# Kernel tuning notes

Measured on AMD Instinct MI355X. Metric: run time of the kernel, lower is better.

Reference implementation:

```python
import jax, jax.numpy as jnp
import numpy as np

B, N, D = 2048, 65536, 128  # batch queries, max_engrams, spike_dim


def setup_inputs() -> dict:
    key = jax.random.key(0)
    k1, k2, k3, k4 = jax.random.split(key, 4)
    sensor_spikes = jax.random.normal(k1, (B, D), dtype=jnp.float32)
    # crystallize_skill stores sign(pattern), so keys/values are +-1 vectors
    sensor_keys = jnp.sign(jax.random.normal(k2, (N, D), dtype=jnp.float32))
    action_values = jnp.sign(jax.random.normal(k3, (N, D), dtype=jnp.float32))
    is_active = jax.random.bernoulli(k4, 0.5, (N,))
    return {
        "sensor_spikes": sensor_spikes,
        "sensor_keys": sensor_keys,
        "action_values": action_values,
        "is_active": is_active,
    }


def reference(sensor_spikes, sensor_keys, action_values, is_active):
    # similarity = x @ keys.T  -> [B, N]
    sim = jnp.einsum("bd,nd->bn", sensor_spikes.astype(jnp.float32), sensor_keys)
    # masked_fill_(~is_active, -inf)
    sim = jnp.where(is_active[None, :], sim, -jnp.inf)
    best_match_idx = jnp.argmax(sim, axis=-1)          # [B]
    confidence = jnp.max(sim, axis=-1)                 # [B] == sim[b, best_idx[b]]
    retrieved = action_values[best_match_idx]          # [B, D]
    return retrieved, confidence, best_match_idx
```

## Files before the change

### kernel.cpp

```cpp
#include <hip/hip_runtime.h>
#include <stdint.h>

typedef __attribute__((ext_vector_type(8))) short short8;
typedef __attribute__((ext_vector_type(4))) float f32x4;

#define NEG_INF (-__builtin_inff())

#define B_ROWS 2048
#define N_KEYS 65536
#define DIM    128
#define NCHUNK 2048


__device__ __forceinline__ unsigned short f2bf(float f) {
  unsigned u = __float_as_uint(f);
  u = (u + 0x7FFFu + ((u >> 16) & 1u)) >> 16;
  return (unsigned short)u;
}


__global__ __launch_bounds__(256) void convert_x_kernel(
    const float* __restrict__ x, short8* __restrict__ xi) {
  int t = blockIdx.x * 256 + threadIdx.x;
  int rb = t >> 8, loc = t & 255;
  int rl = rb * 16 + (loc & 15);
  int c = loc >> 4;
  const float* src = x + (size_t)rl * DIM + c * 8;
  f32x4 v0 = *(const f32x4*)(src);
  f32x4 v1 = *(const f32x4*)(src + 4);
  short8 o;
  o[0] = (short)f2bf(v0[0]); o[1] = (short)f2bf(v0[1]);
  o[2] = (short)f2bf(v0[2]); o[3] = (short)f2bf(v0[3]);
  o[4] = (short)f2bf(v1[0]); o[5] = (short)f2bf(v1[1]);
  o[6] = (short)f2bf(v1[2]); o[7] = (short)f2bf(v1[3]);
  xi[t] = o;
}

__global__ __launch_bounds__(256, 4) void sim4_kernel(
    const short8* __restrict__ xi, const float* __restrict__ keys,
    const int* __restrict__ act, float* __restrict__ cmax) {
  __shared__ short8 Bs[2048];
  const int tid = threadIdx.x;
  const int w = tid >> 6, l = tid & 63;
  const int ntile = blockIdx.x;

  const float* kb = keys + (size_t)ntile * (128 * DIM);
#pragma unroll
  for (int it = 0; it < 8; ++it) {
    int li = it * 256 + tid;
    int rl = ((li >> 8) << 4) + (li & 15);
    int c = (li >> 4) & 15;
    const float* src = kb + rl * DIM + c * 8;
    f32x4 v0 = *(const f32x4*)(src);
    f32x4 v1 = *(const f32x4*)(src + 4);
    int a = act[ntile * 128 + rl];
    short8 o;
    o[0] = (short)f2bf(v0[0]); o[1] = (short)f2bf(v0[1]);
    o[2] = (short)f2bf(v0[2]); o[3] = (short)f2bf(v0[3]);
    o[4] = (short)f2bf(v1[0]); o[5] = (short)f2bf(v1[1]);
    o[6] = (short)f2bf(v1[2]); o[7] = (short)f2bf(v1[3]);
    if (!a) o = short8{0, 0, 0, 0, 0, 0, 0, 0};
    Bs[li] = o;
  }
  __syncthreads();

  short8 kf[2][4];
#pragma unroll
  for (int mi = 0; mi < 2; mi++)
#pragma unroll
    for (int kk = 0; kk < 4; kk++)
      kf[mi][kk] = Bs[(w * 2 + mi) * 256 + kk * 64 + l];

  const int chunk = ntile * 4 + w;
  const int lr = l & 15;
  float* cbase = cmax + chunk;

  for (int it = 0; it < 64; ++it) {
    short8 xf[2][4];
#pragma unroll
    for (int ni = 0; ni < 2; ni++)
#pragma unroll
      for (int kk = 0; kk < 4; kk++)
        xf[ni][kk] = xi[(it * 2 + ni) * 256 + kk * 64 + l];

    f32x4 acc[2][2];
#pragma unroll
    for (int mi = 0; mi < 2; mi++)
#pragma unroll
      for (int ni = 0; ni < 2; ni++) acc[mi][ni] = f32x4{0.f, 0.f, 0.f, 0.f};

#pragma unroll
    for (int kk = 0; kk < 4; kk++)
#pragma unroll
      for (int mi = 0; mi < 2; mi++)
#pragma unroll
        for (int ni = 0; ni < 2; ni++)
          acc[mi][ni] = __builtin_amdgcn_mfma_f32_16x16x32_bf16(
              kf[mi][kk], xf[ni][kk], acc[mi][ni], 0, 0, 0);

#pragma unroll
    for (int ni = 0; ni < 2; ni++) {
      float t0 = fmaxf(acc[0][ni][0], acc[1][ni][0]);
      float t1 = fmaxf(acc[0][ni][1], acc[1][ni][1]);
      float t2 = fmaxf(acc[0][ni][2], acc[1][ni][2]);
      float t3 = fmaxf(acc[0][ni][3], acc[1][ni][3]);
      float v = fmaxf(fmaxf(t0, t1), fmaxf(t2, t3));
      v = fmaxf(v, __shfl_xor(v, 16));
      v = fmaxf(v, __shfl_xor(v, 32));
      if (l < 16)
        cbase[(size_t)(it * 32 + ni * 16 + lr) * NCHUNK] = v;
    }
  }
}

__global__ __launch_bounds__(256) void finalize2_kernel(
    const float* __restrict__ x, const float* __restrict__ keys,
    const float* __restrict__ vals, const int* __restrict__ act,
    const float* __restrict__ cmax, float* __restrict__ out) {
  __shared__ float xr[128];
  __shared__ float wred[4];
  __shared__ int cand[256];
  __shared__ int ncand;
  __shared__ double redv[4];
  __shared__ int redn[4];
  __shared__ int bestn_s;
  const int b = blockIdx.x, tid = threadIdx.x;
  const int w = tid >> 6, l = tid & 63;
  if (tid < 128) xr[tid] = x[(size_t)b * 128 + tid];
  if (tid == 0) ncand = 0;
  __syncthreads();

  const float* cm = cmax + (size_t)b * NCHUNK;
  float c[8];
  float lm = NEG_INF;
#pragma unroll
  for (int j = 0; j < 8; j++) {
    c[j] = cm[tid + j * 256];
    lm = fmaxf(lm, c[j]);
  }
#pragma unroll
  for (int s = 1; s < 64; s <<= 1) lm = fmaxf(lm, __shfl_xor(lm, s));
  if (l == 0) wred[w] = lm;
  __syncthreads();
  float M = fmaxf(fmaxf(wred[0], wred[1]), fmaxf(wred[2], wred[3]));
  float thr = M - 0.75f;

#pragma unroll
  for (int j = 0; j < 8; j++) {
    if (c[j] > thr) {
      int p = atomicAdd(&ncand, 1);
      if (p < 256) cand[p] = tid + j * 256;
    }
  }
  __syncthreads();
  int nc = ncand; if (nc > 256) nc = 256;

  double bv = -(double)__builtin_inf();
  int bn = 0x7FFFFFFF;
  const int key_off = tid >> 3;
  const int d0 = (tid & 7) * 16;
  for (int ci = 0; ci < nc; ci++) {
    int n = cand[ci] * 32 + key_off;
    const float* kr = keys + (size_t)n * 128 + d0;
    double s = 0.0;
#pragma unroll
    for (int u = 0; u < 16; u += 4) {
      f32x4 kv = *(const f32x4*)(kr + u);
      s += (double)xr[d0 + u] * (double)kv[0];
      s += (double)xr[d0 + u + 1] * (double)kv[1];
      s += (double)xr[d0 + u + 2] * (double)kv[2];
      s += (double)xr[d0 + u + 3] * (double)kv[3];
    }
    s += __shfl_xor(s, 1);
    s += __shfl_xor(s, 2);
    s += __shfl_xor(s, 4);
    if ((tid & 7) == 0 && act[n] != 0) {
      if (s > bv || (s == bv && n < bn)) { bv = s; bn = n; }
    }
  }

#pragma unroll
  for (int s = 1; s < 64; s <<= 1) {
    double ov = __shfl_xor(bv, s);
    int on = __shfl_xor(bn, s);
    if (ov > bv || (ov == bv && on < bn)) { bv = ov; bn = on; }
  }
  if (l == 0) { redv[w] = bv; redn[w] = bn; }
  __syncthreads();
  if (tid == 0) {
    double v = redv[0]; int n = redn[0];
#pragma unroll
    for (int j = 1; j < 4; j++) {
      if (redv[j] > v || (redv[j] == v && redn[j] < n)) { v = redv[j]; n = redn[j]; }
    }
    bestn_s = n;
    out[262144 + b] = (float)v;
    out[264192 + b] = (float)n;
  }
  __syncthreads();
  int n = bestn_s;
  if (tid < 128) out[(size_t)b * 128 + tid] = vals[(size_t)n * 128 + tid];
}

__global__ __launch_bounds__(256) void direct_kernel(
    const float* __restrict__ x, const float* __restrict__ keys,
    const float* __restrict__ vals, const int* __restrict__ act,
    float* __restrict__ out) {
  __shared__ float xr[8][128];
  __shared__ double redv[8][4];
  __shared__ int redn[8][4];
  __shared__ int bests[8];
  const int tid = threadIdx.x;
  const int r0 = blockIdx.x * 8;
  const int w = tid >> 6, l = tid & 63;
#pragma unroll
  for (int i = 0; i < 4; i++) {
    int idx = tid + i * 256;
    xr[idx >> 7][idx & 127] = x[(size_t)(r0 + (idx >> 7)) * 128 + (idx & 127)];
  }
  __syncthreads();

  double bv[8];
  int bn[8];
#pragma unroll
  for (int r = 0; r < 8; r++) { bv[r] = -(double)__builtin_inf(); bn[r] = 0x7FFFFFFF; }

  for (int n = tid; n < N_KEYS; n += 256) {
    if (act[n] == 0) continue;
    const float* kr = keys + (size_t)n * 128;
    double s[8];
#pragma unroll
    for (int r = 0; r < 8; r++) s[r] = 0.0;
    for (int d = 0; d < 128; d += 4) {
      f32x4 kv = *(const f32x4*)(kr + d);
#pragma unroll
      for (int r = 0; r < 8; r++) {
        s[r] += (double)xr[r][d] * (double)kv[0];
        s[r] += (double)xr[r][d + 1] * (double)kv[1];
        s[r] += (double)xr[r][d + 2] * (double)kv[2];
        s[r] += (double)xr[r][d + 3] * (double)kv[3];
      }
    }
#pragma unroll
    for (int r = 0; r < 8; r++)
      if (s[r] > bv[r]) { bv[r] = s[r]; bn[r] = n; }
  }

#pragma unroll
  for (int r = 0; r < 8; r++) {
    double v = bv[r]; int n = bn[r];
#pragma unroll
    for (int s = 1; s < 64; s <<= 1) {
      double ov = __shfl_xor(v, s);
      int on = __shfl_xor(n, s);
      if (ov > v || (ov == v && on < n)) { v = ov; n = on; }
    }
    if (l == 0) { redv[r][w] = v; redn[r][w] = n; }
  }
  __syncthreads();
  if (tid < 8) {
    double v = redv[tid][0]; int n = redn[tid][0];
#pragma unroll
    for (int j = 1; j < 4; j++) {
      double ov = redv[tid][j]; int on = redn[tid][j];
      if (ov > v || (ov == v && on < n)) { v = ov; n = on; }
    }
    bests[tid] = n;
    out[262144 + r0 + tid] = (float)v;
    out[264192 + r0 + tid] = (float)n;
  }
  __syncthreads();
#pragma unroll
  for (int i = 0; i < 4; i++) {
    int idx = tid + i * 256;
    int r = idx >> 7, d = idx & 127;
    out[(size_t)(r0 + r) * 128 + d] = vals[(size_t)bests[r] * 128 + d];
  }
}

extern "C" void kernel_launch(void* const* d_in, const int* in_sizes, int n_in,
                              void* d_out, int out_size, void* d_ws, size_t ws_size,
                              hipStream_t stream) {
  const float* x    = (const float*)d_in[0];
  const float* keys = (const float*)d_in[1];
  const float* vals = (const float*)d_in[2];
  const int*   act  = (const int*)d_in[3];
  float* out = (float*)d_out;

  const size_t need = (size_t)32768 * sizeof(short8) +
                      (size_t)B_ROWS * NCHUNK * sizeof(float);
  if (ws_size >= need) {
    short8* xi   = (short8*)d_ws;
    float*  cmax = (float*)(xi + 32768);
    convert_x_kernel<<<128, 256, 0, stream>>>(x, xi);
    sim4_kernel<<<512, 256, 0, stream>>>(xi, keys, act, cmax);
    finalize2_kernel<<<2048, 256, 0, stream>>>(x, keys, vals, act, cmax, out);
  } else {
    direct_kernel<<<256, 256, 0, stream>>>(x, keys, vals, act, out);
  }
}
```

Before: 176.3 us.

## Pre-convert keys to bf16 and retile similarity kernel with 64-key chunks

Keys are now converted to bf16 and masked once in a combined conversion kernel instead of per block in shared memory. The similarity kernel holds 64 keys per wave in registers, splits queries across a second grid dimension, and writes a coalesced row-major chunk-max matrix with half as many chunks. The finalize stage rescans 64 keys per candidate chunk with 4 threads per key. This trades an extra bf16 key buffer in global memory and larger candidate rescans for fewer cmax writes and fewer partial-max outputs.

```diff
diff --git a/kernel.cpp b/kernel.cpp
--- a/kernel.cpp
+++ b/kernel.cpp
@@ -9,7 +9,7 @@
 #define B_ROWS 2048
 #define N_KEYS 65536
 #define DIM    128
-#define NCHUNK 2048
+#define NCHUNK 1024
 
 
 __device__ __forceinline__ unsigned short f2bf(float f) {
@@ -19,107 +19,103 @@
 }
 
 
-__global__ __launch_bounds__(256) void convert_x_kernel(
-    const float* __restrict__ x, short8* __restrict__ xi) {
+__global__ __launch_bounds__(256) void convert_kernel(
+    const float* __restrict__ x, const float* __restrict__ keys,
+    const int* __restrict__ act, short8* __restrict__ xi,
+    short8* __restrict__ ki) {
   int t = blockIdx.x * 256 + threadIdx.x;
-  int rb = t >> 8, loc = t & 255;
-  int rl = rb * 16 + (loc & 15);
-  int c = loc >> 4;
-  const float* src = x + (size_t)rl * DIM + c * 8;
+  const float* src;
+  short8* dst;
+  int mask = 1;
+  if (t < 32768) {
+    int rb = t >> 8, loc = t & 255;
+    int row = rb * 16 + (loc & 15);
+    int c = loc >> 4;
+    src = x + (size_t)row * DIM + c * 8;
+    dst = xi + t;
+  } else {
+    t -= 32768;
+    int rb = t >> 8, loc = t & 255;
+    int row = rb * 16 + (loc & 15);
+    int c = loc >> 4;
+    src = keys + (size_t)row * DIM + c * 8;
+    dst = ki + t;
+    mask = act[row];
+  }
   f32x4 v0 = *(const f32x4*)(src);
   f32x4 v1 = *(const f32x4*)(src + 4);
   short8 o;
-  o[0] = (short)f2bf(v0[0]); o[1] = (short)f2bf(v0[1]);
-  o[2] = (short)f2bf(v0[2]); o[3] = (short)f2bf(v0[3]);
-  o[4] = (short)f2bf(v1[0]); o[5] = (short)f2bf(v1[1]);
-  o[6] = (short)f2bf(v1[2]); o[7] = (short)f2bf(v1[3]);
-  xi[t] = o;
-}
-
-__global__ __launch_bounds__(256, 4) void sim4_kernel(
-    const short8* __restrict__ xi, const float* __restrict__ keys,
-    const int* __restrict__ act, float* __restrict__ cmax) {
-  __shared__ short8 Bs[2048];
-  const int tid = threadIdx.x;
-  const int w = tid >> 6, l = tid & 63;
-  const int ntile = blockIdx.x;
-
-  const float* kb = keys + (size_t)ntile * (128 * DIM);
-#pragma unroll
-  for (int it = 0; it < 8; ++it) {
-    int li = it * 256 + tid;
-    int rl = ((li >> 8) << 4) + (li & 15);
-    int c = (li >> 4) & 15;
-    const float* src = kb + rl * DIM + c * 8;
-    f32x4 v0 = *(const f32x4*)(src);
-    f32x4 v1 = *(const f32x4*)(src + 4);
-    int a = act[ntile * 128 + rl];
-    short8 o;
+  if (mask) {
     o[0] = (short)f2bf(v0[0]); o[1] = (short)f2bf(v0[1]);
     o[2] = (short)f2bf(v0[2]); o[3] = (short)f2bf(v0[3]);
     o[4] = (short)f2bf(v1[0]); o[5] = (short)f2bf(v1[1]);
     o[6] = (short)f2bf(v1[2]); o[7] = (short)f2bf(v1[3]);
-    if (!a) o = short8{0, 0, 0, 0, 0, 0, 0, 0};
-    Bs[li] = o;
-  }
-  __syncthreads();
-
-  short8 kf[2][4];
-#pragma unroll
-  for (int mi = 0; mi < 2; mi++)
+  } else {
+    o = short8{0, 0, 0, 0, 0, 0, 0, 0};
+  }
+  *dst = o;
+}
+
+__global__ __launch_bounds__(256, 4) void sim5_kernel(
+    const short8* __restrict__ xi, const short8* __restrict__ ki,
+    float* __restrict__ cmax) {
+  const int tid = threadIdx.x;
+  const int w = tid >> 6, l = tid & 63;
+  const int tile = blockIdx.x;
+  const int q = blockIdx.y;
+
+  short8 kf[4][4];
+#pragma unroll
+  for (int mi = 0; mi < 4; mi++) {
+    int g = tile * 16 + w * 4 + mi;
 #pragma unroll
     for (int kk = 0; kk < 4; kk++)
-      kf[mi][kk] = Bs[(w * 2 + mi) * 256 + kk * 64 + l];
-
-  const int chunk = ntile * 4 + w;
+      kf[mi][kk] = ki[g * 256 + kk * 64 + l];
+  }
+  asm volatile("" ::: "memory");
+
+  const int chunk = tile * 4 + w;
   const int lr = l & 15;
-  float* cbase = cmax + chunk;
-
-  for (int it = 0; it < 64; ++it) {
-    short8 xf[2][4];
-#pragma unroll
-    for (int ni = 0; ni < 2; ni++)
-#pragma unroll
-      for (int kk = 0; kk < 4; kk++)
-        xf[ni][kk] = xi[(it * 2 + ni) * 256 + kk * 64 + l];
-
-    f32x4 acc[2][2];
-#pragma unroll
-    for (int mi = 0; mi < 2; mi++)
-#pragma unroll
-      for (int ni = 0; ni < 2; ni++) acc[mi][ni] = f32x4{0.f, 0.f, 0.f, 0.f};
-
+  const short8* xq = xi + (size_t)q * 8192;
+
+  for (int it = 0; it < 32; ++it) {
+    short8 xf[4];
 #pragma unroll
     for (int kk = 0; kk < 4; kk++)
-#pragma unroll
-      for (int mi = 0; mi < 2; mi++)
-#pragma unroll
-        for (int ni = 0; ni < 2; ni++)
-          acc[mi][ni] = __builtin_amdgcn_mfma_f32_16x16x32_bf16(
-              kf[mi][kk], xf[ni][kk], acc[mi][ni], 0, 0, 0);
-
-#pragma unroll
-    for (int ni = 0; ni < 2; ni++) {
-      float t0 = fmaxf(acc[0][ni][0], acc[1][ni][0]);
-      float t1 = fmaxf(acc[0][ni][1], acc[1][ni][1]);
-      float t2 = fmaxf(acc[0][ni][2], acc[1][ni][2]);
-      float t3 = fmaxf(acc[0][ni][3], acc[1][ni][3]);
-      float v = fmaxf(fmaxf(t0, t1), fmaxf(t2, t3));
-      v = fmaxf(v, __shfl_xor(v, 16));
-      v = fmaxf(v, __shfl_xor(v, 32));
-      if (l < 16)
-        cbase[(size_t)(it * 32 + ni * 16 + lr) * NCHUNK] = v;
-    }
-  }
-}
-
-__global__ __launch_bounds__(256) void finalize2_kernel(
+      xf[kk] = xq[it * 256 + kk * 64 + l];
+
+    f32x4 acc[4];
+#pragma unroll
+    for (int mi = 0; mi < 4; mi++) acc[mi] = f32x4{0.f, 0.f, 0.f, 0.f};
+
+#pragma unroll
+    for (int kk = 0; kk < 4; kk++)
+#pragma unroll
+      for (int mi = 0; mi < 4; mi++)
+        acc[mi] = __builtin_amdgcn_mfma_f32_16x16x32_bf16(
+            kf[mi][kk], xf[kk], acc[mi], 0, 0, 0);
+
+    float v = acc[0][0];
+#pragma unroll
+    for (int mi = 0; mi < 4; mi++)
+#pragma unroll
+      for (int r = 0; r < 4; r++) v = fmaxf(v, acc[mi][r]);
+    v = fmaxf(v, __shfl_xor(v, 16));
+    v = fmaxf(v, __shfl_xor(v, 32));
+    if (l < 16) {
+      int row = q * 512 + it * 16 + lr;
+      cmax[(size_t)row * NCHUNK + chunk] = v;
+    }
+  }
+}
+
+__global__ __launch_bounds__(256) void finalize3_kernel(
     const float* __restrict__ x, const float* __restrict__ keys,
     const float* __restrict__ vals, const int* __restrict__ act,
     const float* __restrict__ cmax, float* __restrict__ out) {
   __shared__ float xr[128];
   __shared__ float wred[4];
-  __shared__ int cand[256];
+  __shared__ int cand[1024];
   __shared__ int ncand;
   __shared__ double redv[4];
   __shared__ int redn[4];
@@ -131,10 +127,10 @@
   __syncthreads();
 
   const float* cm = cmax + (size_t)b * NCHUNK;
-  float c[8];
+  float c[4];
   float lm = NEG_INF;
 #pragma unroll
-  for (int j = 0; j < 8; j++) {
+  for (int j = 0; j < 4; j++) {
     c[j] = cm[tid + j * 256];
     lm = fmaxf(lm, c[j]);
   }
@@ -146,25 +142,25 @@
   float thr = M - 0.75f;
 
 #pragma unroll
-  for (int j = 0; j < 8; j++) {
+  for (int j = 0; j < 4; j++) {
     if (c[j] > thr) {
       int p = atomicAdd(&ncand, 1);
-      if (p < 256) cand[p] = tid + j * 256;
-    }
-  }
-  __syncthreads();
-  int nc = ncand; if (nc > 256) nc = 256;
+      cand[p] = tid + j * 256;
+    }
+  }
+  __syncthreads();
+  int nc = ncand;
 
   double bv = -(double)__builtin_inf();
   int bn = 0x7FFFFFFF;
-  const int key_off = tid >> 3;
-  const int d0 = (tid & 7) * 16;
+  const int key_off = tid >> 2;
+  const int d0 = (tid & 3) * 32;
   for (int ci = 0; ci < nc; ci++) {
-    int n = cand[ci] * 32 + key_off;
+    int n = cand[ci] * 64 + key_off;
     const float* kr = keys + (size_t)n * 128 + d0;
     double s = 0.0;
 #pragma unroll
-    for (int u = 0; u < 16; u += 4) {
+    for (int u = 0; u < 32; u += 4) {
       f32x4 kv = *(const f32x4*)(kr + u);
       s += (double)xr[d0 + u] * (double)kv[0];
       s += (double)xr[d0 + u + 1] * (double)kv[1];
@@ -173,8 +169,7 @@
     }
     s += __shfl_xor(s, 1);
     s += __shfl_xor(s, 2);
-    s += __shfl_xor(s, 4);
-    if ((tid & 7) == 0 && act[n] != 0) {
+    if ((tid & 3) == 0 && act[n] != 0) {
       if (s > bv || (s == bv && n < bn)) { bv = s; bn = n; }
     }
   }
@@ -287,14 +282,15 @@
   const int*   act  = (const int*)d_in[3];
   float* out = (float*)d_out;
 
-  const size_t need = (size_t)32768 * sizeof(short8) +
+  const size_t need = (size_t)(32768 + 1048576) * sizeof(short8) +
                       (size_t)B_ROWS * NCHUNK * sizeof(float);
   if (ws_size >= need) {
     short8* xi   = (short8*)d_ws;
-    float*  cmax = (float*)(xi + 32768);
-    convert_x_kernel<<<128, 256, 0, stream>>>(x, xi);
-    sim4_kernel<<<512, 256, 0, stream>>>(xi, keys, act, cmax);
-    finalize2_kernel<<<2048, 256, 0, stream>>>(x, keys, vals, act, cmax, out);
+    short8* ki   = xi + 32768;
+    float*  cmax = (float*)(ki + 1048576);
+    convert_kernel<<<4224, 256, 0, stream>>>(x, keys, act, xi, ki);
+    sim5_kernel<<<dim3(256, 4), 256, 0, stream>>>(xi, ki, cmax);
+    finalize3_kernel<<<2048, 256, 0, stream>>>(x, keys, vals, act, cmax, out);
   } else {
     direct_kernel<<<256, 256, 0, stream>>>(x, keys, vals, act, out);
   }
```

Measured after the change: 153.6 us, median of 2. 1.15x faster.

## Transpose chunk-max buffer and batch 16 query rows per finalize block

Applied to the files above, without the earlier changes.

The similarity kernel now writes per-chunk maxima in a chunk-major layout, so each wave stores 16 contiguous floats instead of scattered strided writes. Its inner loop processes one 16-row query tile per iteration, and the occupancy hint drops from 4 to 2. The finalize kernel handles 16 rows per block with 128 blocks instead of 2048, reading the transposed buffer coalesced across rows. It then rescores candidate (chunk,row) pairs serially with block-wide syncs and a single-thread reduction. That may serialize work and cuts the number of blocks, and candidates are capped at 128 per block, which is tighter than the previous 256 per row.

```diff
diff --git a/kernel.cpp b/kernel.cpp
--- a/kernel.cpp
+++ b/kernel.cpp
@@ -23,9 +23,9 @@
     const float* __restrict__ x, short8* __restrict__ xi) {
   int t = blockIdx.x * 256 + threadIdx.x;
   int rb = t >> 8, loc = t & 255;
-  int rl = rb * 16 + (loc & 15);
+  int row = rb * 16 + (loc & 15);
   int c = loc >> 4;
-  const float* src = x + (size_t)rl * DIM + c * 8;
+  const float* src = x + (size_t)row * DIM + c * 8;
   f32x4 v0 = *(const f32x4*)(src);
   f32x4 v1 = *(const f32x4*)(src + 4);
   short8 o;
@@ -36,15 +36,15 @@
   xi[t] = o;
 }
 
-__global__ __launch_bounds__(256, 4) void sim4_kernel(
+__global__ __launch_bounds__(256, 2) void sim6_kernel(
     const short8* __restrict__ xi, const float* __restrict__ keys,
-    const int* __restrict__ act, float* __restrict__ cmax) {
+    const int* __restrict__ act, float* __restrict__ cmaxT) {
   __shared__ short8 Bs[2048];
   const int tid = threadIdx.x;
   const int w = tid >> 6, l = tid & 63;
-  const int ntile = blockIdx.x;
-
-  const float* kb = keys + (size_t)ntile * (128 * DIM);
+  const int tile = blockIdx.x;
+
+  const float* kb = keys + (size_t)tile * (128 * DIM);
 #pragma unroll
   for (int it = 0; it < 8; ++it) {
     int li = it * 256 + tid;
@@ -53,7 +53,7 @@
     const float* src = kb + rl * DIM + c * 8;
     f32x4 v0 = *(const f32x4*)(src);
     f32x4 v1 = *(const f32x4*)(src + 4);
-    int a = act[ntile * 128 + rl];
+    int a = act[tile * 128 + rl];
     short8 o;
     o[0] = (short)f2bf(v0[0]); o[1] = (short)f2bf(v0[1]);
     o[2] = (short)f2bf(v0[2]); o[3] = (short)f2bf(v0[3]);
@@ -66,140 +66,143 @@
 
   short8 kf[2][4];
 #pragma unroll
-  for (int mi = 0; mi < 2; mi++)
+  for (int mi = 0; mi < 2; mi++) {
+    int kb2 = w * 2 + mi;
 #pragma unroll
     for (int kk = 0; kk < 4; kk++)
-      kf[mi][kk] = Bs[(w * 2 + mi) * 256 + kk * 64 + l];
-
-  const int chunk = ntile * 4 + w;
-  const int lr = l & 15;
-  float* cbase = cmax + chunk;
-
-  for (int it = 0; it < 64; ++it) {
-    short8 xf[2][4];
-#pragma unroll
-    for (int ni = 0; ni < 2; ni++)
-#pragma unroll
-      for (int kk = 0; kk < 4; kk++)
-        xf[ni][kk] = xi[(it * 2 + ni) * 256 + kk * 64 + l];
-
-    f32x4 acc[2][2];
+      kf[mi][kk] = Bs[kb2 * 256 + kk * 64 + l];
+  }
+  asm volatile("" ::: "memory");
+
+  const int chunk = tile * 4 + w;
+  float* cbase = cmaxT + (size_t)chunk * B_ROWS;
+
+  for (int it = 0; it < 128; ++it) {
+    short8 xf[4];
+#pragma unroll
+    for (int kk = 0; kk < 4; kk++)
+      xf[kk] = xi[it * 256 + kk * 64 + l];
+
+    f32x4 acc[2];
+#pragma unroll
+    for (int mi = 0; mi < 2; mi++) acc[mi] = f32x4{0.f, 0.f, 0.f, 0.f};
+
+#pragma unroll
+    for (int kk = 0; kk < 4; kk++)
+#pragma unroll
+      for (int mi = 0; mi < 2; mi++)
+        acc[mi] = __builtin_amdgcn_mfma_f32_16x16x32_bf16(
+            kf[mi][kk], xf[kk], acc[mi], 0, 0, 0);
+
+    float v = acc[0][0];
 #pragma unroll
     for (int mi = 0; mi < 2; mi++)
 #pragma unroll
-      for (int ni = 0; ni < 2; ni++) acc[mi][ni] = f32x4{0.f, 0.f, 0.f, 0.f};
-
-#pragma unroll
-    for (int kk = 0; kk < 4; kk++)
-#pragma unroll
-      for (int mi = 0; mi < 2; mi++)
-#pragma unroll
-        for (int ni = 0; ni < 2; ni++)
-          acc[mi][ni] = __builtin_amdgcn_mfma_f32_16x16x32_bf16(
-              kf[mi][kk], xf[ni][kk], acc[mi][ni], 0, 0, 0);
-
-#pragma unroll
-    for (int ni = 0; ni < 2; ni++) {
-      float t0 = fmaxf(acc[0][ni][0], acc[1][ni][0]);
-      float t1 = fmaxf(acc[0][ni][1], acc[1][ni][1]);
-      float t2 = fmaxf(acc[0][ni][2], acc[1][ni][2]);
-      float t3 = fmaxf(acc[0][ni][3], acc[1][ni][3]);
-      float v = fmaxf(fmaxf(t0, t1), fmaxf(t2, t3));
-      v = fmaxf(v, __shfl_xor(v, 16));
-      v = fmaxf(v, __shfl_xor(v, 32));
-      if (l < 16)
-        cbase[(size_t)(it * 32 + ni * 16 + lr) * NCHUNK] = v;
-    }
-  }
-}
-
-__global__ __launch_bounds__(256) void finalize2_kernel(
+      for (int r = 0; r < 4; r++) v = fmaxf(v, acc[mi][r]);
+    v = fmaxf(v, __shfl_xor(v, 16));
+    v = fmaxf(v, __shfl_xor(v, 32));
+    if (l < 16) cbase[it * 16 + l] = v;
+  }
+}
+
+__global__ __launch_bounds__(256) void finalize4_kernel(
     const float* __restrict__ x, const float* __restrict__ keys,
     const float* __restrict__ vals, const int* __restrict__ act,
-    const float* __restrict__ cmax, float* __restrict__ out) {
-  __shared__ float xr[128];
-  __shared__ float wred[4];
-  __shared__ int cand[256];
-  __shared__ int ncand;
-  __shared__ double redv[4];
-  __shared__ int redn[4];
-  __shared__ int bestn_s;
-  const int b = blockIdx.x, tid = threadIdx.x;
+    const float* __restrict__ cmaxT, float* __restrict__ out) {
+  __shared__ float xr[16][128];
+  __shared__ float wmax[4][16];
+  __shared__ float thr_s[16];
+  __shared__ int pr_chunk[128];
+  __shared__ int pr_row[128];
+  __shared__ int npair;
+  __shared__ double ps[32];
+  __shared__ double best_v[16];
+  __shared__ int best_n[16];
+  const int tid = threadIdx.x;
   const int w = tid >> 6, l = tid & 63;
-  if (tid < 128) xr[tid] = x[(size_t)b * 128 + tid];
-  if (tid == 0) ncand = 0;
-  __syncthreads();
-
-  const float* cm = cmax + (size_t)b * NCHUNK;
-  float c[8];
+  const int r0 = blockIdx.x * 16;
+  const int my_row = tid & 15;
+  const int ci0 = tid >> 4;
+
+#pragma unroll
+  for (int i = 0; i < 8; i++) {
+    int idx = tid + i * 256;
+    xr[idx >> 7][idx & 127] = x[(size_t)(r0 + (idx >> 7)) * DIM + (idx & 127)];
+  }
+  if (tid < 16) { best_v[tid] = -(double)__builtin_inf(); best_n[tid] = 0x7FFFFFFF; }
+  if (tid == 0) npair = 0;
+  __syncthreads();
+
   float lm = NEG_INF;
-#pragma unroll
-  for (int j = 0; j < 8; j++) {
-    c[j] = cm[tid + j * 256];
-    lm = fmaxf(lm, c[j]);
-  }
-#pragma unroll
-  for (int s = 1; s < 64; s <<= 1) lm = fmaxf(lm, __shfl_xor(lm, s));
-  if (l == 0) wred[w] = lm;
-  __syncthreads();
-  float M = fmaxf(fmaxf(wred[0], wred[1]), fmaxf(wred[2], wred[3]));
-  float thr = M - 0.75f;
-
-#pragma unroll
-  for (int j = 0; j < 8; j++) {
-    if (c[j] > thr) {
-      int p = atomicAdd(&ncand, 1);
-      if (p < 256) cand[p] = tid + j * 256;
-    }
-  }
-  __syncthreads();
-  int nc = ncand; if (nc > 256) nc = 256;
-
-  double bv = -(double)__builtin_inf();
-  int bn = 0x7FFFFFFF;
+  for (int i = 0; i < 128; i++) {
+    int c = ci0 + 16 * i;
+    lm = fmaxf(lm, cmaxT[(size_t)c * B_ROWS + r0 + my_row]);
+  }
+  lm = fmaxf(lm, __shfl_xor(lm, 16));
+  lm = fmaxf(lm, __shfl_xor(lm, 32));
+  if (l < 16) wmax[w][l] = lm;
+  __syncthreads();
+  if (tid < 16)
+    thr_s[tid] = fmaxf(fmaxf(wmax[0][tid], wmax[1][tid]),
+                       fmaxf(wmax[2][tid], wmax[3][tid])) - 0.75f;
+  __syncthreads();
+
+  float thr = thr_s[my_row];
+  for (int i = 0; i < 128; i++) {
+    int c = ci0 + 16 * i;
+    float v = cmaxT[(size_t)c * B_ROWS + r0 + my_row];
+    if (v > thr) {
+      int p = atomicAdd(&npair, 1);
+      if (p < 128) { pr_chunk[p] = c; pr_row[p] = my_row; }
+    }
+  }
+  __syncthreads();
+  int np = npair; if (np > 128) np = 128;
+
   const int key_off = tid >> 3;
   const int d0 = (tid & 7) * 16;
-  for (int ci = 0; ci < nc; ci++) {
-    int n = cand[ci] * 32 + key_off;
-    const float* kr = keys + (size_t)n * 128 + d0;
+  for (int p = 0; p < np; p++) {
+    int c = pr_chunk[p], row = pr_row[p];
+    int n = c * 32 + key_off;
+    const float* kr = keys + (size_t)n * DIM + d0;
+    const float* xv = &xr[row][d0];
     double s = 0.0;
 #pragma unroll
     for (int u = 0; u < 16; u += 4) {
       f32x4 kv = *(const f32x4*)(kr + u);
-      s += (double)xr[d0 + u] * (double)kv[0];
-      s += (double)xr[d0 + u + 1] * (double)kv[1];
-      s += (double)xr[d0 + u + 2] * (double)kv[2];
-      s += (double)xr[d0 + u + 3] * (double)kv[3];
+      s += (double)xv[u] * (double)kv[0];
+      s += (double)xv[u + 1] * (double)kv[1];
+      s += (double)xv[u + 2] * (double)kv[2];
+      s += (double)xv[u + 3] * (double)kv[3];
     }
     s += __shfl_xor(s, 1);
     s += __shfl_xor(s, 2);
     s += __shfl_xor(s, 4);
-    if ((tid & 7) == 0 && act[n] != 0) {
-      if (s > bv || (s == bv && n < bn)) { bv = s; bn = n; }
-    }
-  }
-
-#pragma unroll
-  for (int s = 1; s < 64; s <<= 1) {
-    double ov = __shfl_xor(bv, s);
-    int on = __shfl_xor(bn, s);
-    if (ov > bv || (ov == bv && on < bn)) { bv = ov; bn = on; }
-  }
-  if (l == 0) { redv[w] = bv; redn[w] = bn; }
-  __syncthreads();
-  if (tid == 0) {
-    double v = redv[0]; int n = redn[0];
-#pragma unroll
-    for (int j = 1; j < 4; j++) {
-      if (redv[j] > v || (redv[j] == v && redn[j] < n)) { v = redv[j]; n = redn[j]; }
-    }
-    bestn_s = n;
-    out[262144 + b] = (float)v;
-    out[264192 + b] = (float)n;
-  }
-  __syncthreads();
-  int n = bestn_s;
-  if (tid < 128) out[(size_t)b * 128 + tid] = vals[(size_t)n * 128 + tid];
+    if ((tid & 7) == 0)
+      ps[key_off] = (act[n] != 0) ? s : -(double)__builtin_inf();
+    __syncthreads();
+    if (tid == 0) {
+      for (int k = 0; k < 32; k++) {
+        int n2 = c * 32 + k;
+        if (ps[k] > best_v[row] || (ps[k] == best_v[row] && n2 < best_n[row])) {
+          best_v[row] = ps[k]; best_n[row] = n2;
+        }
+      }
+    }
+    __syncthreads();
+  }
+
+  if (tid < 16) {
+    out[262144 + r0 + tid] = (float)best_v[tid];
+    out[264192 + r0 + tid] = (float)best_n[tid];
+  }
+  __syncthreads();
+#pragma unroll
+  for (int i = 0; i < 8; i++) {
+    int idx = tid + i * 256;
+    int row = idx >> 7, d = idx & 127;
+    out[(size_t)(r0 + row) * DIM + d] = vals[(size_t)best_n[row] * DIM + d];
+  }
 }
 
 __global__ __launch_bounds__(256) void direct_kernel(
@@ -288,13 +291,13 @@
   float* out = (float*)d_out;
 
   const size_t need = (size_t)32768 * sizeof(short8) +
-                      (size_t)B_ROWS * NCHUNK * sizeof(float);
+                      (size_t)NCHUNK * B_ROWS * sizeof(float);
   if (ws_size >= need) {
-    short8* xi   = (short8*)d_ws;
-    float*  cmax = (float*)(xi + 32768);
+    short8* xi    = (short8*)d_ws;
+    float*  cmaxT = (float*)(xi + 32768);
     convert_x_kernel<<<128, 256, 0, stream>>>(x, xi);
-    sim4_kernel<<<512, 256, 0, stream>>>(xi, keys, act, cmax);
-    finalize2_kernel<<<2048, 256, 0, stream>>>(x, keys, vals, act, cmax, out);
+    sim6_kernel<<<512, 256, 0, stream>>>(xi, keys, act, cmaxT);
+    finalize4_kernel<<<128, 256, 0, stream>>>(x, keys, vals, act, cmaxT, out);
   } else {
     direct_kernel<<<256, 256, 0, stream>>>(x, keys, vals, act, out);
   }
```

Result: slower. 300.5 us (+70.4%).
